# Kernel optimization log

Hardware: AMD Instinct MI355X
Metric: run time of the kernel (lower is better)

The kernel has to match this reference:

```python
import jax, jax.numpy as jnp
import numpy as np

N, C, H, E = 4096, 512, 8, 131072
D = C // H
ALPHA = 0.5
EPS = 1e-5


def layer_norm(x, g, b):
    mu = jnp.mean(x, axis=-1, keepdims=True)
    var = jnp.mean((x - mu) ** 2, axis=-1, keepdims=True)
    return (x - mu) * jax.lax.rsqrt(var + EPS) * g + b


def setup_inputs() -> dict:
    key = jax.random.key(0)
    ks = jax.random.split(key, 20)
    s = 0.02
    return {
        "x": jax.random.normal(ks[0], (N, C), jnp.float32),
        "edge_index": jax.random.randint(ks[1], (2, E), 0, N, jnp.int32),
        "local_w": jax.random.normal(ks[2], (C, C), jnp.float32) * s,
        "local_b": jnp.zeros((C,), jnp.float32),
        "in_proj_w": jax.random.normal(ks[3], (3 * C, C), jnp.float32) * s,
        "in_proj_b": jnp.zeros((3 * C,), jnp.float32),
        "attn_out_w": jax.random.normal(ks[4], (C, C), jnp.float32) * s,
        "attn_out_b": jnp.zeros((C,), jnp.float32),
        "output_w": jax.random.normal(ks[5], (C, C), jnp.float32) * s,
        "output_b": jnp.zeros((C,), jnp.float32),
        "norm1_g": jnp.ones((C,), jnp.float32),
        "norm1_b": jnp.zeros((C,), jnp.float32),
        "norm2_g": jnp.ones((C,), jnp.float32),
        "norm2_b": jnp.zeros((C,), jnp.float32),
        "ffn_w1": jax.random.normal(ks[6], (2 * C, C), jnp.float32) * s,
        "ffn_b1": jnp.zeros((2 * C,), jnp.float32),
        "ffn_w2": jax.random.normal(ks[7], (C, 2 * C), jnp.float32) * s,
        "ffn_b2": jnp.zeros((C,), jnp.float32),
    }


def reference(x, edge_index, local_w, local_b, in_proj_w, in_proj_b,
              attn_out_w, attn_out_b, output_w, output_b,
              norm1_g, norm1_b, norm2_g, norm2_b,
              ffn_w1, ffn_b1, ffn_w2, ffn_b2):
    src, dst = edge_index[0], edge_index[1]

    # local branch: linear then scatter-mean over incoming edges
    local_h = x @ local_w.T + local_b                       # [N,C]
    summed = jax.ops.segment_sum(local_h[src], dst, num_segments=N)
    cnt = jax.ops.segment_sum(jnp.ones((E,), x.dtype), dst, num_segments=N)
    local_out = summed / jnp.maximum(cnt, 1.0)[:, None]

    # global branch: full self-attention over all nodes
    qkv = x @ in_proj_w.T + in_proj_b                       # [N,3C]
    q, k, v = jnp.split(qkv, 3, axis=-1)
    q = q.reshape(N, H, D)
    k = k.reshape(N, H, D)
    v = v.reshape(N, H, D)
    scores = jnp.einsum('nhd,mhd->hnm', q, k) / jnp.sqrt(jnp.asarray(D, x.dtype))
    attn = jax.nn.softmax(scores, axis=-1)                  # [H,N,N]
    ctx = jnp.einsum('hnm,mhd->nhd', attn, v).reshape(N, C)
    global_out = ctx @ attn_out_w.T + attn_out_b

    mixed = ALPHA * local_out + (1.0 - ALPHA) * global_out
    hidden = layer_norm(x + (mixed @ output_w.T + output_b), norm1_g, norm1_b)

    ff = jax.nn.gelu(hidden @ ffn_w1.T + ffn_b1, approximate=False) @ ffn_w2.T + ffn_b2
    return layer_norm(hidden + ff, norm2_g, norm2_b)
```

## Files before the change

kernel.cpp:

```cpp
#include <hip/hip_runtime.h>


#define N_NODES 4096
#define C_DIM   512
#define H_HEADS 8
#define D_HEAD  64
#define E_EDGES 131072

typedef unsigned short u16;
typedef unsigned int   u32;
typedef u16   u16x8  __attribute__((ext_vector_type(8)));
typedef __bf16 bf16x8 __attribute__((ext_vector_type(8)));
typedef float  f32x4  __attribute__((ext_vector_type(4)));

__device__ __forceinline__ float b2f(u16 u) {
  unsigned int i = ((unsigned int)u) << 16;
  return __builtin_bit_cast(float, i);
}
__device__ __forceinline__ u16 f2b(float f) {
  unsigned int i = __builtin_bit_cast(unsigned int, f);
  i += 0x7fffu + ((i >> 16) & 1u);
  return (u16)(i >> 16);
}
__device__ __forceinline__ u16 f2b_up(float f) {
  unsigned int i = __builtin_bit_cast(unsigned int, f);
  return (u16)((i + 0x8000u) >> 16);
}

struct CvtArgs {
  const float* src[7];
  u16* dst[7];
  int n[7];
  const int* ei;
  int* deg;
};

__global__ __launch_bounds__(256) void cvt_multi(CvtArgs a) {
  const int t = blockIdx.y;
  if (t == 7) {
    if (blockIdx.x >= E_EDGES / 256) return;
    const int e = blockIdx.x * 256 + threadIdx.x;
    atomicAdd(&a.deg[a.ei[E_EDGES + e]], 1);
    return;
  }
  const int i = (blockIdx.x * 256 + threadIdx.x) * 8;
  if (i >= a.n[t]) return;
  const float* s = a.src[t] + i;
  f32x4 v0 = *(const f32x4*)s;
  f32x4 v1 = *(const f32x4*)(s + 4);
  u16x8 o;
  o[0]=f2b(v0[0]); o[1]=f2b(v0[1]); o[2]=f2b(v0[2]); o[3]=f2b(v0[3]);
  o[4]=f2b(v1[0]); o[5]=f2b(v1[1]); o[6]=f2b(v1[2]); o[7]=f2b(v1[3]);
  *(u16x8*)(a.dst[t] + i) = o;
}

template<int EPI>
__global__ __launch_bounds__(256) void gemm_bt(
    const u16* __restrict__ A, const u16* __restrict__ W,
    const float* __restrict__ bias, void* __restrict__ outp,
    int M, int Nout, int K,
    const float* __restrict__ mloc)
{
  const int tid  = threadIdx.x;
  const int lane = tid & 63, wave = tid >> 6;
  const int quad = lane >> 4, l16 = lane & 15;
  const int wm = wave >> 1, wn = wave & 1;
  const int bm = blockIdx.x, bnb = blockIdx.y;

  __shared__ __align__(16) u16 As[64][72];
  __shared__ __align__(16) u16 Ws[64][72];

  f32x4 acc[2][2] = {};

  const int srow = tid >> 2;
  const int scol = (tid & 3) << 4;
  const u16* ag = A + (size_t)(bm  * 64 + srow) * K + scol;
  const u16* wg = W + (size_t)(bnb * 64 + srow) * K + scol;

  for (int k0 = 0; k0 < K; k0 += 64) {
    u16x8 a0 = *(const u16x8*)(ag + k0);
    u16x8 a1 = *(const u16x8*)(ag + k0 + 8);
    u16x8 w0 = *(const u16x8*)(wg + k0);
    u16x8 w1 = *(const u16x8*)(wg + k0 + 8);
    __syncthreads();
    *(u16x8*)&As[srow][scol]     = a0;
    *(u16x8*)&As[srow][scol + 8] = a1;
    *(u16x8*)&Ws[srow][scol]     = w0;
    *(u16x8*)&Ws[srow][scol + 8] = w1;
    __syncthreads();
#pragma unroll
    for (int ks = 0; ks < 2; ++ks) {
      bf16x8 af[2], bf[2];
      af[0] = *(const bf16x8*)&As[wm * 32 +      l16][ks * 32 + quad * 8];
      af[1] = *(const bf16x8*)&As[wm * 32 + 16 + l16][ks * 32 + quad * 8];
      bf[0] = *(const bf16x8*)&Ws[wn * 32 +      l16][ks * 32 + quad * 8];
      bf[1] = *(const bf16x8*)&Ws[wn * 32 + 16 + l16][ks * 32 + quad * 8];
#pragma unroll
      for (int i = 0; i < 2; ++i)
#pragma unroll
        for (int j = 0; j < 2; ++j)
          acc[i][j] = __builtin_amdgcn_mfma_f32_16x16x32_bf16(af[i], bf[j], acc[i][j], 0, 0, 0);
    }
  }

#pragma unroll
  for (int i = 0; i < 2; ++i)
#pragma unroll
    for (int j = 0; j < 2; ++j) {
      const int col = bnb * 64 + wn * 32 + j * 16 + l16;
      const float bias_v = bias[col];
#pragma unroll
      for (int r = 0; r < 4; ++r) {
        const int row = bm * 64 + wm * 32 + i * 16 + quad * 4 + r;
        float v = acc[i][j][r] + bias_v;
        const size_t o = (size_t)row * Nout + col;
        if constexpr (EPI == 1) {
          ((float*)outp)[o] = v;
        } else {
          ((u16*)outp)[o] = f2b(0.5f * mloc[o] + 0.5f * v);
        }
      }
    }
}

template<int MODE>
__global__ __launch_bounds__(256) void gemm128(
    const u16* __restrict__ A, const u16* __restrict__ W,
    const float* __restrict__ bias0, const float* __restrict__ bias1,
    u16* __restrict__ out0, u16* __restrict__ out1,
    int M, int Nout, int K)
{
  const int tid  = threadIdx.x;
  const int lane = tid & 63, wave = tid >> 6;
  const int quad = lane >> 4, l16 = lane & 15;
  const int wm = wave >> 1, wn = wave & 1;
  const int bm = blockIdx.x, bnb = blockIdx.y;

  __shared__ __align__(16) u16 As[128][72];
  __shared__ __align__(16) u16 Ws[128][72];

  f32x4 acc[4][4] = {};

  const int srow = tid >> 1;
  const int scol = (tid & 1) * 32;
  const u16* ag = A + (size_t)(bm  * 128 + srow) * K + scol;
  const u16* wg = W + (size_t)(bnb * 128 + srow) * K + scol;

  for (int k0 = 0; k0 < K; k0 += 64) {
    u16x8 a0 = *(const u16x8*)(ag + k0);
    u16x8 a1 = *(const u16x8*)(ag + k0 + 8);
    u16x8 a2 = *(const u16x8*)(ag + k0 + 16);
    u16x8 a3 = *(const u16x8*)(ag + k0 + 24);
    u16x8 w0 = *(const u16x8*)(wg + k0);
    u16x8 w1 = *(const u16x8*)(wg + k0 + 8);
    u16x8 w2 = *(const u16x8*)(wg + k0 + 16);
    u16x8 w3 = *(const u16x8*)(wg + k0 + 24);
    __syncthreads();
    *(u16x8*)&As[srow][scol]      = a0;
    *(u16x8*)&As[srow][scol + 8]  = a1;
    *(u16x8*)&As[srow][scol + 16] = a2;
    *(u16x8*)&As[srow][scol + 24] = a3;
    *(u16x8*)&Ws[srow][scol]      = w0;
    *(u16x8*)&Ws[srow][scol + 8]  = w1;
    *(u16x8*)&Ws[srow][scol + 16] = w2;
    *(u16x8*)&Ws[srow][scol + 24] = w3;
    __syncthreads();
#pragma unroll
    for (int ks = 0; ks < 2; ++ks) {
      bf16x8 af[4], bf[4];
#pragma unroll
      for (int am = 0; am < 4; ++am)
        af[am] = *(const bf16x8*)&As[wm * 64 + am * 16 + l16][ks * 32 + quad * 8];
#pragma unroll
      for (int bn = 0; bn < 4; ++bn)
        bf[bn] = *(const bf16x8*)&Ws[wn * 64 + bn * 16 + l16][ks * 32 + quad * 8];
#pragma unroll
      for (int am = 0; am < 4; ++am)
#pragma unroll
        for (int bn = 0; bn < 4; ++bn)
          acc[am][bn] = __builtin_amdgcn_mfma_f32_16x16x32_bf16(af[am], bf[bn], acc[am][bn], 0, 0, 0);
    }
  }

#pragma unroll
  for (int am = 0; am < 4; ++am)
#pragma unroll
    for (int bn = 0; bn < 4; ++bn) {
      const int col = bnb * 128 + wn * 64 + bn * 16 + l16;
      float bias_v;
      if constexpr (MODE == 0) bias_v = (col < 512) ? bias0[col] : bias1[col - 512];
      else                     bias_v = bias0[col];
#pragma unroll
      for (int r = 0; r < 4; ++r) {
        const int row = bm * 128 + wm * 64 + am * 16 + quad * 4 + r;
        float v = acc[am][bn][r] + bias_v;
        if constexpr (MODE == 0) {
          if (col < 512) out0[(size_t)row * 512 + col] = f2b(v);
          else           out1[(size_t)row * 1536 + (col - 512)] = f2b(v);
        } else {
          float gl = 0.5f * v * (1.0f + erff(v * 0.70710678118654752f));
          out0[(size_t)row * Nout + col] = f2b(gl);
        }
      }
    }
}

__global__ __launch_bounds__(256) void scan_kernel(
    const int* __restrict__ deg, int* __restrict__ off, int* __restrict__ cursor)
{
  __shared__ int part[256];
  const int t = threadIdx.x;
  int v[16];
  int s = 0;
#pragma unroll
  for (int i = 0; i < 16; ++i) { v[i] = deg[t * 16 + i]; s += v[i]; }
  part[t] = s;
  __syncthreads();
  for (int d = 1; d < 256; d <<= 1) {
    int val = (t >= d) ? part[t - d] : 0;
    __syncthreads();
    if (t >= d) part[t] += val;
    __syncthreads();
  }
  int prefix = (t == 0) ? 0 : part[t - 1];
#pragma unroll
  for (int i = 0; i < 16; ++i) {
    off[t * 16 + i] = prefix;
    cursor[t * 16 + i] = prefix;
    prefix += v[i];
  }
  if (t == 255) off[4096] = prefix;
}

__global__ __launch_bounds__(256) void fill_kernel(
    const int* __restrict__ ei, int* __restrict__ cursor, int* __restrict__ csr)
{
  const int e = blockIdx.x * 256 + threadIdx.x;
  const int s = ei[e];
  const int d = ei[E_EDGES + e];
  const int p = atomicAdd(&cursor[d], 1);
  csr[p] = s;
}

__global__ __launch_bounds__(256) void gather_kernel(
    const int* __restrict__ off, const int* __restrict__ csr,
    const u16* __restrict__ lh, float* __restrict__ lo)
{
  const int wave = threadIdx.x >> 6, lane = threadIdx.x & 63;
  const int n = blockIdx.x * 4 + wave;
  const int j0 = off[n], j1 = off[n + 1];
  float acc[8] = {};
  for (int j = j0; j < j1; ++j) {
    const int s = csr[j];
    const u16x8 v = *(const u16x8*)(lh + (size_t)s * C_DIM + lane * 8);
#pragma unroll
    for (int i = 0; i < 8; ++i) acc[i] += b2f(v[i]);
  }
  const float inv = 1.0f / fmaxf((float)(j1 - j0), 1.0f);
  f32x4 o0, o1;
#pragma unroll
  for (int i = 0; i < 4; ++i) { o0[i] = acc[i] * inv; o1[i] = acc[4 + i] * inv; }
  float* op = lo + (size_t)n * C_DIM + lane * 8;
  *(f32x4*)op = o0;
  *(f32x4*)(op + 4) = o1;
}

__global__ __launch_bounds__(256) void vtrans_kernel(
    const u16* __restrict__ qkv, u16* __restrict__ vt)
{
  const int tid = threadIdx.x;
  const int d = tid & 63, mg = tid >> 6;
  const int h = blockIdx.y, mt = blockIdx.x;
  const int m0 = mt * 64 + mg * 16;
  u16 buf[16];
#pragma unroll
  for (int i = 0; i < 16; ++i)
    buf[i] = qkv[(size_t)(m0 + i) * 1536 + 1024 + h * 64 + d];
  u16x8 w0, w1;
#pragma unroll
  for (int i = 0; i < 8; ++i) { w0[i] = buf[i]; w1[i] = buf[8 + i]; }
  u16* op = vt + (size_t)(h * 64 + d) * N_NODES + m0;
  *(u16x8*)op = w0;
  *(u16x8*)(op + 8) = w1;
}

template<int SPLITS>
__global__ __launch_bounds__(256) void attn_kernel(
    const u16* __restrict__ qkv, const u16* __restrict__ vt,
    float* __restrict__ opart, float* __restrict__ lpart)
{
  const int tid = threadIdx.x, wave = tid >> 6, lane = tid & 63;
  const int quad = lane >> 4, l16 = lane & 15;
  const int h = blockIdx.y, tile = blockIdx.x, split = blockIdx.z;

  __shared__ __align__(16) u16 Ks[64][72];
  __shared__ __align__(16) u16 Vts[64][72];
  __shared__ __align__(16) u16 Ps[128][72];

  const float QSCALE = 0.18033688011112042f;
  bf16x8 aq[2][2];
#pragma unroll
  for (int mb = 0; mb < 2; ++mb) {
    const int qrow = tile * 128 + wave * 32 + mb * 16 + l16;
    const u16* qp = qkv + (size_t)qrow * 1536 + h * 64 + quad * 8;
    u16x8 q0 = *(const u16x8*)qp;
    u16x8 q1 = *(const u16x8*)(qp + 32);
    u16x8 s0, s1;
#pragma unroll
    for (int i = 0; i < 8; ++i) {
      s0[i] = f2b(b2f(q0[i]) * QSCALE);
      s1[i] = f2b(b2f(q1[i]) * QSCALE);
    }
    aq[mb][0] = __builtin_bit_cast(bf16x8, s0);
    aq[mb][1] = __builtin_bit_cast(bf16x8, s1);
  }

  f32x4 O[2][4] = {};
  float lsum[2][4] = {};

  const int srow = tid >> 2;
  const int scol = (tid & 3) << 4;

  const int mt1 = (split + 1) * (64 / SPLITS);
  for (int mt = split * (64 / SPLITS); mt < mt1; ++mt) {
    const u16* kp = qkv + (size_t)(mt * 64 + srow) * 1536 + 512 + h * 64 + scol;
    const u16* vp = vt + (size_t)(h * 64 + srow) * N_NODES + mt * 64 + scol;
    u16x8 k0 = *(const u16x8*)kp;
    u16x8 k1 = *(const u16x8*)(kp + 8);
    u16x8 v0 = *(const u16x8*)vp;
    u16x8 v1 = *(const u16x8*)(vp + 8);
    __syncthreads();
    *(u16x8*)&Ks[srow][scol]      = k0;
    *(u16x8*)&Ks[srow][scol + 8]  = k1;
    *(u16x8*)&Vts[srow][scol]     = v0;
    *(u16x8*)&Vts[srow][scol + 8] = v1;
    __syncthreads();

    f32x4 s[2][4] = {};
#pragma unroll
    for (int ks = 0; ks < 2; ++ks) {
      bf16x8 bk[4];
#pragma unroll
      for (int jn = 0; jn < 4; ++jn)
        bk[jn] = *(const bf16x8*)&Ks[jn * 16 + l16][ks * 32 + quad * 8];
#pragma unroll
      for (int mb = 0; mb < 2; ++mb)
#pragma unroll
        for (int jn = 0; jn < 4; ++jn)
          s[mb][jn] = __builtin_amdgcn_mfma_f32_16x16x32_bf16(aq[mb][ks], bk[jn], s[mb][jn], 0, 0, 0);
    }

#pragma unroll
    for (int mb = 0; mb < 2; ++mb)
#pragma unroll
      for (int jn = 0; jn < 4; ++jn)
#pragma unroll
        for (int r = 0; r < 4; ++r) {
          float p = __builtin_amdgcn_exp2f(s[mb][jn][r]);
          lsum[mb][r] += p;
          Ps[wave * 32 + mb * 16 + quad * 4 + r][jn * 16 + l16] = f2b_up(p);
        }

#pragma unroll
    for (int ks = 0; ks < 2; ++ks) {
      bf16x8 bv[4];
#pragma unroll
      for (int jd = 0; jd < 4; ++jd)
        bv[jd] = *(const bf16x8*)&Vts[jd * 16 + l16][ks * 32 + quad * 8];
#pragma unroll
      for (int mb = 0; mb < 2; ++mb) {
        bf16x8 ap = *(const bf16x8*)&Ps[wave * 32 + mb * 16 + l16][ks * 32 + quad * 8];
#pragma unroll
        for (int jd = 0; jd < 4; ++jd)
          O[mb][jd] = __builtin_amdgcn_mfma_f32_16x16x32_bf16(ap, bv[jd], O[mb][jd], 0, 0, 0);
      }
    }
  }

#pragma unroll
  for (int mb = 0; mb < 2; ++mb)
#pragma unroll
    for (int r = 0; r < 4; ++r)
#pragma unroll
      for (int off = 1; off < 16; off <<= 1)
        lsum[mb][r] += __shfl_xor(lsum[mb][r], off);

#pragma unroll
  for (int mb = 0; mb < 2; ++mb)
#pragma unroll
    for (int r = 0; r < 4; ++r) {
      const int row = tile * 128 + wave * 32 + mb * 16 + quad * 4 + r;
      float* orow = opart + ((size_t)split * N_NODES + row) * C_DIM + h * 64;
#pragma unroll
      for (int jd = 0; jd < 4; ++jd)
        orow[jd * 16 + l16] = O[mb][jd][r];
      if (l16 == 0)
        lpart[((size_t)split * N_NODES + row) * H_HEADS + h] = lsum[mb][r];
    }
}

template<int SPLITS>
__global__ __launch_bounds__(256) void attn_combine(
    const float* __restrict__ opart, const float* __restrict__ lpart,
    u16* __restrict__ ctx)
{
  const size_t base = (size_t)(blockIdx.x * 256 + threadIdx.x) * 8;
  const int row = (int)(base >> 9);
  const int h = (int)((base & 511) >> 6);
  float l = 0.0f;
#pragma unroll
  for (int s = 0; s < SPLITS; ++s)
    l += lpart[(size_t)s * N_NODES * H_HEADS + (size_t)row * H_HEADS + h];
  const float inv = 1.0f / l;
  float o[8] = {};
#pragma unroll
  for (int s = 0; s < SPLITS; ++s) {
    const float* op = opart + (size_t)s * N_NODES * C_DIM + base;
    f32x4 p0 = *(const f32x4*)op;
    f32x4 p1 = *(const f32x4*)(op + 4);
#pragma unroll
    for (int i = 0; i < 4; ++i) { o[i] += p0[i]; o[4 + i] += p1[i]; }
  }
  u16x8 ob;
#pragma unroll
  for (int i = 0; i < 8; ++i) ob[i] = f2b(o[i] * inv);
  *(u16x8*)(ctx + base) = ob;
}

__global__ __launch_bounds__(256) void ln1_kernel(
    const float* __restrict__ x, const float* __restrict__ pr,
    const float* __restrict__ g, const float* __restrict__ b,
    u16* __restrict__ hb, float* __restrict__ hf)
{
  const int wave = threadIdx.x >> 6, lane = threadIdx.x & 63;
  const int row = blockIdx.x * 4 + wave;
  const int c0 = lane * 8;
  const size_t base = (size_t)row * C_DIM + c0;
  f32x4 x0 = *(const f32x4*)(x + base);
  f32x4 x1 = *(const f32x4*)(x + base + 4);
  f32x4 p0 = *(const f32x4*)(pr + base);
  f32x4 p1 = *(const f32x4*)(pr + base + 4);
  float v[8];
#pragma unroll
  for (int i = 0; i < 4; ++i) { v[i] = x0[i] + p0[i]; v[4 + i] = x1[i] + p1[i]; }
  float sum = 0, sq = 0;
#pragma unroll
  for (int i = 0; i < 8; ++i) { sum += v[i]; sq += v[i] * v[i]; }
  for (int off = 1; off < 64; off <<= 1) { sum += __shfl_xor(sum, off); sq += __shfl_xor(sq, off); }
  const float mean = sum * (1.0f / C_DIM);
  const float var  = sq * (1.0f / C_DIM) - mean * mean;
  const float rstd = rsqrtf(var + 1e-5f);
  f32x4 g0 = *(const f32x4*)(g + c0), g1 = *(const f32x4*)(g + c0 + 4);
  f32x4 b0 = *(const f32x4*)(b + c0), b1 = *(const f32x4*)(b + c0 + 4);
  u16x8 ob; f32x4 h0, h1;
#pragma unroll
  for (int i = 0; i < 4; ++i) {
    float hv0 = (v[i]     - mean) * rstd * g0[i] + b0[i];
    float hv1 = (v[4 + i] - mean) * rstd * g1[i] + b1[i];
    h0[i] = hv0; h1[i] = hv1;
    ob[i] = f2b(hv0); ob[4 + i] = f2b(hv1);
  }
  *(u16x8*)(hb + base) = ob;
  *(f32x4*)(hf + base) = h0;
  *(f32x4*)(hf + base + 4) = h1;
}

__global__ __launch_bounds__(256) void ln2_kernel(
    const float* __restrict__ a, const float* __restrict__ c,
    const float* __restrict__ g, const float* __restrict__ b,
    float* __restrict__ out)
{
  const int wave = threadIdx.x >> 6, lane = threadIdx.x & 63;
  const int row = blockIdx.x * 4 + wave;
  const int c0 = lane * 8;
  const size_t base = (size_t)row * C_DIM + c0;
  f32x4 a0 = *(const f32x4*)(a + base), a1 = *(const f32x4*)(a + base + 4);
  f32x4 c0v = *(const f32x4*)(c + base), c1v = *(const f32x4*)(c + base + 4);
  float v[8];
#pragma unroll
  for (int i = 0; i < 4; ++i) { v[i] = a0[i] + c0v[i]; v[4 + i] = a1[i] + c1v[i]; }
  float sum = 0, sq = 0;
#pragma unroll
  for (int i = 0; i < 8; ++i) { sum += v[i]; sq += v[i] * v[i]; }
  for (int off = 1; off < 64; off <<= 1) { sum += __shfl_xor(sum, off); sq += __shfl_xor(sq, off); }
  const float mean = sum * (1.0f / C_DIM);
  const float var  = sq * (1.0f / C_DIM) - mean * mean;
  const float rstd = rsqrtf(var + 1e-5f);
  f32x4 g0 = *(const f32x4*)(g + c0), g1 = *(const f32x4*)(g + c0 + 4);
  f32x4 b0 = *(const f32x4*)(b + c0), b1 = *(const f32x4*)(b + c0 + 4);
  f32x4 h0, h1;
#pragma unroll
  for (int i = 0; i < 4; ++i) {
    h0[i] = (v[i]     - mean) * rstd * g0[i] + b0[i];
    h1[i] = (v[4 + i] - mean) * rstd * g1[i] + b1[i];
  }
  *(f32x4*)(out + base) = h0;
  *(f32x4*)(out + base + 4) = h1;
}

extern "C" void kernel_launch(void* const* d_in, const int* in_sizes, int n_in,
                              void* d_out, int out_size, void* d_ws, size_t ws_size,
                              hipStream_t stream) {
  const float* x          = (const float*)d_in[0];
  const int*   ei         = (const int*)d_in[1];
  const float* local_w    = (const float*)d_in[2];
  const float* local_b    = (const float*)d_in[3];
  const float* in_proj_w  = (const float*)d_in[4];
  const float* in_proj_b  = (const float*)d_in[5];
  const float* attn_out_w = (const float*)d_in[6];
  const float* attn_out_b = (const float*)d_in[7];
  const float* output_w   = (const float*)d_in[8];
  const float* output_b   = (const float*)d_in[9];
  const float* n1g = (const float*)d_in[10];
  const float* n1b = (const float*)d_in[11];
  const float* n2g = (const float*)d_in[12];
  const float* n2b = (const float*)d_in[13];
  const float* ffn_w1 = (const float*)d_in[14];
  const float* ffn_b1 = (const float*)d_in[15];
  const float* ffn_w2 = (const float*)d_in[16];
  const float* ffn_b2 = (const float*)d_in[17];
  float* out = (float*)d_out;

  char* ws = (char*)d_ws;
  size_t o = 0;
  float* local_out = (float*)(ws + o); o += (size_t)N_NODES * C_DIM * 4;
  int* deg    = (int*)(ws + o); o += (N_NODES) * 4;
  int* off    = (int*)(ws + o); o += (N_NODES + 16) * 4;
  int* cursor = (int*)(ws + o); o += (N_NODES) * 4;
  int* csr    = (int*)(ws + o); o += (size_t)E_EDGES * 4;
  u16* xb   = (u16*)(ws + o); o += (size_t)N_NODES * C_DIM * 2;
  u16* wbLQ = (u16*)(ws + o); o += (size_t)4 * C_DIM * C_DIM * 2;
  u16* wbA  = (u16*)(ws + o); o += (size_t)C_DIM * C_DIM * 2;
  u16* wbO  = (u16*)(ws + o); o += (size_t)C_DIM * C_DIM * 2;
  u16* wbF1 = (u16*)(ws + o); o += (size_t)2 * C_DIM * C_DIM * 2;
  u16* wbF2 = (u16*)(ws + o); o += (size_t)2 * C_DIM * C_DIM * 2;
  u16* local_h   = (u16*)(ws + o); o += (size_t)N_NODES * C_DIM * 2;
  u16* qkvb      = (u16*)(ws + o); o += (size_t)N_NODES * 3 * C_DIM * 2;
  u16* ctxb      = (u16*)(ws + o); o += (size_t)N_NODES * C_DIM * 2;
  u16* mixed     = (u16*)(ws + o); o += (size_t)N_NODES * C_DIM * 2;
  u16* hidden_bf = (u16*)(ws + o); o += (size_t)N_NODES * C_DIM * 2;
  float* hidden_f = (float*)(ws + o); o += (size_t)N_NODES * C_DIM * 4;
  u16* ff1       = (u16*)(ws + o); o += (size_t)N_NODES * 2 * C_DIM * 2;
  float* proj  = (float*)qkvb;
  float* ff2   = (float*)local_out;
  u16*   vt    = xb;
  float* opart4 = (float*)(ws + o);
  float* lpart4 = (float*)(ws + o + (size_t)4 * N_NODES * C_DIM * 4);
  const size_t need4 = o + (size_t)4 * N_NODES * C_DIM * 4 + (size_t)4 * N_NODES * H_HEADS * 4;
  const bool use4 = (ws_size >= need4);
  float* opart2 = (float*)hidden_bf;
  float* lpart2 = opart2 + (size_t)2 * N_NODES * C_DIM;

  (void)hipMemsetAsync(deg, 0, N_NODES * 4, stream);

  CvtArgs ca;
  ca.src[0] = x;          ca.dst[0] = xb;   ca.n[0] = N_NODES * C_DIM;
  ca.src[1] = local_w;    ca.dst[1] = wbLQ;                  ca.n[1] = C_DIM * C_DIM;
  ca.src[2] = in_proj_w;  ca.dst[2] = wbLQ + C_DIM * C_DIM;  ca.n[2] = 3 * C_DIM * C_DIM;
  ca.src[3] = attn_out_w; ca.dst[3] = wbA;  ca.n[3] = C_DIM * C_DIM;
  ca.src[4] = output_w;   ca.dst[4] = wbO;  ca.n[4] = C_DIM * C_DIM;
  ca.src[5] = ffn_w1;     ca.dst[5] = wbF1; ca.n[5] = 2 * C_DIM * C_DIM;
  ca.src[6] = ffn_w2;     ca.dst[6] = wbF2; ca.n[6] = 2 * C_DIM * C_DIM;
  ca.ei = ei; ca.deg = deg;
  cvt_multi<<<dim3(N_NODES * C_DIM / 2048, 8), 256, 0, stream>>>(ca);

  scan_kernel<<<1, 256, 0, stream>>>(deg, off, cursor);
  fill_kernel<<<E_EDGES / 256, 256, 0, stream>>>(ei, cursor, csr);

  gemm128<0><<<dim3(32, 16), 256, 0, stream>>>(xb, wbLQ, local_b, in_proj_b,
      local_h, qkvb, N_NODES, 4 * C_DIM, C_DIM);
  gather_kernel<<<N_NODES / 4, 256, 0, stream>>>(off, csr, local_h, local_out);

  vtrans_kernel<<<dim3(64, 8), 256, 0, stream>>>(qkvb, vt);
  if (use4) {
    attn_kernel<4><<<dim3(32, 8, 4), 256, 0, stream>>>(qkvb, vt, opart4, lpart4);
    attn_combine<4><<<N_NODES * C_DIM / 2048, 256, 0, stream>>>(opart4, lpart4, ctxb);
  } else {
    attn_kernel<2><<<dim3(32, 8, 2), 256, 0, stream>>>(qkvb, vt, opart2, lpart2);
    attn_combine<2><<<N_NODES * C_DIM / 2048, 256, 0, stream>>>(opart2, lpart2, ctxb);
  }

  gemm_bt<3><<<dim3(64, 8), 256, 0, stream>>>(ctxb, wbA, attn_out_b, mixed,
      N_NODES, C_DIM, C_DIM, local_out);

  gemm_bt<1><<<dim3(64, 8), 256, 0, stream>>>(mixed, wbO, output_b, proj,
      N_NODES, C_DIM, C_DIM, nullptr);
  ln1_kernel<<<N_NODES / 4, 256, 0, stream>>>(x, proj, n1g, n1b, hidden_bf, hidden_f);

  gemm128<2><<<dim3(32, 8), 256, 0, stream>>>(hidden_bf, wbF1, ffn_b1, nullptr,
      ff1, nullptr, N_NODES, 2 * C_DIM, C_DIM);
  gemm_bt<1><<<dim3(64, 8), 256, 0, stream>>>(ff1, wbF2, ffn_b2, ff2,
      N_NODES, C_DIM, 2 * C_DIM, nullptr);
  ln2_kernel<<<N_NODES / 4, 256, 0, stream>>>(hidden_f, ff2, n2g, n2b, out);
}
```

Baseline: 295.8 us.

## Load GEMM and attention tiles directly to LDS with XOR-swizzled layout

Global-to-shared tile staging in both GEMM kernels and the attention kernel now uses global_load_lds direct-to-LDS transfers instead of going through registers. The padded shared arrays are replaced by unpadded 64-wide rows with an XOR swizzle on 16-byte chunks so that MFMA fragment reads avoid bank conflicts. The aim is to save VGPRs and the register round trip for staging. No wait on the async load counter is added before the barrier, so correctness relies on the compiler inserting the vmcnt wait, and there is still no double buffering.

```diff
diff --git a/kernel.cpp b/kernel.cpp
--- a/kernel.cpp
+++ b/kernel.cpp
@@ -25,6 +25,11 @@
 __device__ __forceinline__ u16 f2b_up(float f) {
   unsigned int i = __builtin_bit_cast(unsigned int, f);
   return (u16)((i + 0x8000u) >> 16);
+}
+__device__ __forceinline__ void glds16(const u16* g, u16* l) {
+  __builtin_amdgcn_global_load_lds(
+      (const __attribute__((address_space(1))) void*)g,
+      (__attribute__((address_space(3))) void*)l, 16, 0, 0);
 }
 
 struct CvtArgs {
@@ -67,34 +72,33 @@
   const int wm = wave >> 1, wn = wave & 1;
   const int bm = blockIdx.x, bnb = blockIdx.y;
 
-  __shared__ __align__(16) u16 As[64][72];
-  __shared__ __align__(16) u16 Ws[64][72];
+  __shared__ __align__(16) u16 As[64][64];
+  __shared__ __align__(16) u16 Ws[64][64];
 
   f32x4 acc[2][2] = {};
 
-  const int srow = tid >> 2;
-  const int scol = (tid & 3) << 4;
-  const u16* ag = A + (size_t)(bm  * 64 + srow) * K + scol;
-  const u16* wg = W + (size_t)(bnb * 64 + srow) * K + scol;
+  const int lr = lane >> 3, gs = lane & 7;
+  const int g8 = (gs ^ lr) * 8;
+  const u16* a0 = A + (size_t)(bm  * 64 + wave * 16 +     lr) * K + g8;
+  const u16* a1 = A + (size_t)(bm  * 64 + wave * 16 + 8 + lr) * K + g8;
+  const u16* w0 = W + (size_t)(bnb * 64 + wave * 16 +     lr) * K + g8;
+  const u16* w1 = W + (size_t)(bnb * 64 + wave * 16 + 8 + lr) * K + g8;
 
   for (int k0 = 0; k0 < K; k0 += 64) {
-    u16x8 a0 = *(const u16x8*)(ag + k0);
-    u16x8 a1 = *(const u16x8*)(ag + k0 + 8);
-    u16x8 w0 = *(const u16x8*)(wg + k0);
-    u16x8 w1 = *(const u16x8*)(wg + k0 + 8);
-    __syncthreads();
-    *(u16x8*)&As[srow][scol]     = a0;
-    *(u16x8*)&As[srow][scol + 8] = a1;
-    *(u16x8*)&Ws[srow][scol]     = w0;
-    *(u16x8*)&Ws[srow][scol + 8] = w1;
+    __syncthreads();
+    glds16(a0 + k0, &As[wave * 16][0]);
+    glds16(a1 + k0, &As[wave * 16 + 8][0]);
+    glds16(w0 + k0, &Ws[wave * 16][0]);
+    glds16(w1 + k0, &Ws[wave * 16 + 8][0]);
     __syncthreads();
 #pragma unroll
     for (int ks = 0; ks < 2; ++ks) {
+      const int slot = ((ks * 4 + quad) ^ (l16 & 7)) * 8;
       bf16x8 af[2], bf[2];
-      af[0] = *(const bf16x8*)&As[wm * 32 +      l16][ks * 32 + quad * 8];
-      af[1] = *(const bf16x8*)&As[wm * 32 + 16 + l16][ks * 32 + quad * 8];
-      bf[0] = *(const bf16x8*)&Ws[wn * 32 +      l16][ks * 32 + quad * 8];
-      bf[1] = *(const bf16x8*)&Ws[wn * 32 + 16 + l16][ks * 32 + quad * 8];
+      af[0] = *(const bf16x8*)&As[wm * 32 +      l16][slot];
+      af[1] = *(const bf16x8*)&As[wm * 32 + 16 + l16][slot];
+      bf[0] = *(const bf16x8*)&Ws[wn * 32 +      l16][slot];
+      bf[1] = *(const bf16x8*)&Ws[wn * 32 + 16 + l16][slot];
 #pragma unroll
       for (int i = 0; i < 2; ++i)
 #pragma unroll
@@ -136,44 +140,34 @@
   const int wm = wave >> 1, wn = wave & 1;
   const int bm = blockIdx.x, bnb = blockIdx.y;
 
-  __shared__ __align__(16) u16 As[128][72];
-  __shared__ __align__(16) u16 Ws[128][72];
+  __shared__ __align__(16) u16 As[128][64];
+  __shared__ __align__(16) u16 Ws[128][64];
 
   f32x4 acc[4][4] = {};
 
-  const int srow = tid >> 1;
-  const int scol = (tid & 1) * 32;
-  const u16* ag = A + (size_t)(bm  * 128 + srow) * K + scol;
-  const u16* wg = W + (size_t)(bnb * 128 + srow) * K + scol;
+  const int lr = lane >> 3, gs = lane & 7;
+  const int g8 = (gs ^ lr) * 8;
+  const u16* ab = A + (size_t)(bm  * 128 + wave * 32 + lr) * K + g8;
+  const u16* wb = W + (size_t)(bnb * 128 + wave * 32 + lr) * K + g8;
 
   for (int k0 = 0; k0 < K; k0 += 64) {
-    u16x8 a0 = *(const u16x8*)(ag + k0);
-    u16x8 a1 = *(const u16x8*)(ag + k0 + 8);
-    u16x8 a2 = *(const u16x8*)(ag + k0 + 16);
-    u16x8 a3 = *(const u16x8*)(ag + k0 + 24);
-    u16x8 w0 = *(const u16x8*)(wg + k0);
-    u16x8 w1 = *(const u16x8*)(wg + k0 + 8);
-    u16x8 w2 = *(const u16x8*)(wg + k0 + 16);
-    u16x8 w3 = *(const u16x8*)(wg + k0 + 24);
-    __syncthreads();
-    *(u16x8*)&As[srow][scol]      = a0;
-    *(u16x8*)&As[srow][scol + 8]  = a1;
-    *(u16x8*)&As[srow][scol + 16] = a2;
-    *(u16x8*)&As[srow][scol + 24] = a3;
-    *(u16x8*)&Ws[srow][scol]      = w0;
-    *(u16x8*)&Ws[srow][scol + 8]  = w1;
-    *(u16x8*)&Ws[srow][scol + 16] = w2;
-    *(u16x8*)&Ws[srow][scol + 24] = w3;
+    __syncthreads();
+#pragma unroll
+    for (int c = 0; c < 4; ++c) {
+      glds16(ab + (size_t)(c * 8) * K + k0, &As[wave * 32 + c * 8][0]);
+      glds16(wb + (size_t)(c * 8) * K + k0, &Ws[wave * 32 + c * 8][0]);
+    }
     __syncthreads();
 #pragma unroll
     for (int ks = 0; ks < 2; ++ks) {
+      const int slot = ((ks * 4 + quad) ^ (l16 & 7)) * 8;
       bf16x8 af[4], bf[4];
 #pragma unroll
       for (int am = 0; am < 4; ++am)
-        af[am] = *(const bf16x8*)&As[wm * 64 + am * 16 + l16][ks * 32 + quad * 8];
+        af[am] = *(const bf16x8*)&As[wm * 64 + am * 16 + l16][slot];
 #pragma unroll
       for (int bn = 0; bn < 4; ++bn)
-        bf[bn] = *(const bf16x8*)&Ws[wn * 64 + bn * 16 + l16][ks * 32 + quad * 8];
+        bf[bn] = *(const bf16x8*)&Ws[wn * 64 + bn * 16 + l16][slot];
 #pragma unroll
       for (int am = 0; am < 4; ++am)
 #pragma unroll
@@ -293,8 +287,8 @@
   const int quad = lane >> 4, l16 = lane & 15;
   const int h = blockIdx.y, tile = blockIdx.x, split = blockIdx.z;
 
-  __shared__ __align__(16) u16 Ks[64][72];
-  __shared__ __align__(16) u16 Vts[64][72];
+  __shared__ __align__(16) u16 Ks[64][64];
+  __shared__ __align__(16) u16 Vts[64][64];
   __shared__ __align__(16) u16 Ps[128][72];
 
   const float QSCALE = 0.18033688011112042f;
@@ -318,31 +312,27 @@
   f32x4 O[2][4] = {};
   float lsum[2][4] = {};
 
-  const int srow = tid >> 2;
-  const int scol = (tid & 3) << 4;
+  const int lr = lane >> 3, gs = lane & 7;
+  const int g8 = (gs ^ lr) * 8;
+  const int R0 = wave * 16 + lr;
 
   const int mt1 = (split + 1) * (64 / SPLITS);
   for (int mt = split * (64 / SPLITS); mt < mt1; ++mt) {
-    const u16* kp = qkv + (size_t)(mt * 64 + srow) * 1536 + 512 + h * 64 + scol;
-    const u16* vp = vt + (size_t)(h * 64 + srow) * N_NODES + mt * 64 + scol;
-    u16x8 k0 = *(const u16x8*)kp;
-    u16x8 k1 = *(const u16x8*)(kp + 8);
-    u16x8 v0 = *(const u16x8*)vp;
-    u16x8 v1 = *(const u16x8*)(vp + 8);
-    __syncthreads();
-    *(u16x8*)&Ks[srow][scol]      = k0;
-    *(u16x8*)&Ks[srow][scol + 8]  = k1;
-    *(u16x8*)&Vts[srow][scol]     = v0;
-    *(u16x8*)&Vts[srow][scol + 8] = v1;
+    __syncthreads();
+    glds16(qkv + (size_t)(mt * 64 + R0)     * 1536 + 512 + h * 64 + g8, &Ks[wave * 16][0]);
+    glds16(qkv + (size_t)(mt * 64 + R0 + 8) * 1536 + 512 + h * 64 + g8, &Ks[wave * 16 + 8][0]);
+    glds16(vt + (size_t)(h * 64 + R0)     * N_NODES + mt * 64 + g8, &Vts[wave * 16][0]);
+    glds16(vt + (size_t)(h * 64 + R0 + 8) * N_NODES + mt * 64 + g8, &Vts[wave * 16 + 8][0]);
     __syncthreads();
 
     f32x4 s[2][4] = {};
 #pragma unroll
     for (int ks = 0; ks < 2; ++ks) {
+      const int slot = ((ks * 4 + quad) ^ (l16 & 7)) * 8;
       bf16x8 bk[4];
 #pragma unroll
       for (int jn = 0; jn < 4; ++jn)
-        bk[jn] = *(const bf16x8*)&Ks[jn * 16 + l16][ks * 32 + quad * 8];
+        bk[jn] = *(const bf16x8*)&Ks[jn * 16 + l16][slot];
 #pragma unroll
       for (int mb = 0; mb < 2; ++mb)
 #pragma unroll
@@ -363,10 +353,11 @@
 
 #pragma unroll
     for (int ks = 0; ks < 2; ++ks) {
+      const int slot = ((ks * 4 + quad) ^ (l16 & 7)) * 8;
       bf16x8 bv[4];
 #pragma unroll
       for (int jd = 0; jd < 4; ++jd)
-        bv[jd] = *(const bf16x8*)&Vts[jd * 16 + l16][ks * 32 + quad * 8];
+        bv[jd] = *(const bf16x8*)&Vts[jd * 16 + l16][slot];
 #pragma unroll
       for (int mb = 0; mb < 2; ++mb) {
         bf16x8 ap = *(const bf16x8*)&Ps[wave * 32 + mb * 16 + l16][ks * 32 + quad * 8];
```

After: 290.3 us. About the same (-1.9%).
